# Optimization experiments

Hardware: AMD Instinct MI355X
Metric: run time of the kernel (lower is better)

Reference implementation:

```python
import jax, jax.numpy as jnp
import numpy as np

LRELU = 0.01
EPS = 1e-5
HEADS = 4


def _ln(x, g, b):
    m = x.mean(-1, keepdims=True)
    v = ((x - m) ** 2).mean(-1, keepdims=True)
    return (x - m) / jnp.sqrt(v + EPS) * g + b


def _mapx(x, w1, b1, g1, be1, w2, b2, g2, be2, w3, b3):
    h = jax.nn.leaky_relu(_ln(x @ w1 + b1, g1, be1), LRELU)
    h = jax.nn.leaky_relu(_ln(h @ w2 + b2, g2, be2), LRELU)
    return h @ w3 + b3


def _mcab(x, y, wq, bq, wk, bk, wv, bv, wo, bo, rescale):
    # spectral (channel-wise) multi-head cross attention: q from x, k/v from y
    b, c, h, w = x.shape
    n = h * w
    xt = x.reshape(b, c, n).transpose(0, 2, 1)  # (b, n, c)
    yt = y.reshape(b, c, n).transpose(0, 2, 1)
    dh = c // HEADS
    q = (xt @ wq + bq).reshape(b, n, HEADS, dh).transpose(0, 2, 3, 1)  # (b,H,dh,n)
    k = (yt @ wk + bk).reshape(b, n, HEADS, dh).transpose(0, 2, 3, 1)
    v = (yt @ wv + bv).reshape(b, n, HEADS, dh).transpose(0, 2, 3, 1)
    q = q / (jnp.linalg.norm(q, axis=-1, keepdims=True) + 1e-8)
    k = k / (jnp.linalg.norm(k, axis=-1, keepdims=True) + 1e-8)
    attn = jax.nn.softmax(jnp.einsum('bhdn,bhen->bhde', q, k) * rescale, axis=-1)  # (b,H,dh,dh)
    out = jnp.einsum('bhde,bhen->bhdn', attn, v)  # (b,H,dh,n)
    out = out.transpose(0, 3, 1, 2).reshape(b, n, c) @ wo + bo
    out = out + xt  # residual
    return out.transpose(0, 2, 1).reshape(b, c, h, w)


def setup_inputs() -> dict:
    key = jax.random.key(0)
    ks = jax.random.split(key, 16)
    B, C, H, W, K = 4, 64, 128, 128, 21
    s = 0.02
    nrm = lambda k, shape: jax.random.normal(k, shape, jnp.float32) * s
    return {
        'x': jax.random.normal(ks[0], (B, C, H, W), jnp.float32),
        'semantic': jax.random.uniform(ks[1], (B, K, H, W), jnp.float32),
        'wa': nrm(ks[2], (1, C, 4)), 'ba': jnp.zeros((1, 4), jnp.float32),
        'wb': nrm(ks[3], (20, C, 3)), 'bb': jnp.zeros((20, 3), jnp.float32),
        'in_w': nrm(ks[4], (C, C)), 'in_b': jnp.zeros((C,), jnp.float32),
        'mx_w1': nrm(ks[5], (C, 2 * C)), 'mx_b1': jnp.zeros((2 * C,), jnp.float32),
        'mx_g1': jnp.ones((2 * C,), jnp.float32), 'mx_be1': jnp.zeros((2 * C,), jnp.float32),
        'mx_w2': nrm(ks[6], (2 * C, 2 * C)), 'mx_b2': jnp.zeros((2 * C,), jnp.float32),
        'mx_g2': jnp.ones((2 * C,), jnp.float32), 'mx_be2': jnp.zeros((2 * C,), jnp.float32),
        'mx_w3': nrm(ks[7], (2 * C, C)), 'mx_b3': jnp.zeros((C,), jnp.float32),
        'wq': nrm(ks[8], (C, C)), 'bq': jnp.zeros((C,), jnp.float32),
        'wk': nrm(ks[9], (C, C)), 'bk': jnp.zeros((C,), jnp.float32),
        'wv': nrm(ks[10], (C, C)), 'bv': jnp.zeros((C,), jnp.float32),
        'wo': nrm(ks[11], (C, C)), 'bo': jnp.zeros((C,), jnp.float32),
        'rescale': jnp.ones((HEADS, 1, 1), jnp.float32),
    }


def reference(x, semantic, wa, ba, wb, bb, in_w, in_b,
              mx_w1, mx_b1, mx_g1, mx_be1, mx_w2, mx_b2, mx_g2, mx_be2,
              mx_w3, mx_b3, wq, bq, wk, bk, wv, bv, wo, bo, rescale):
    sem = jax.nn.relu(semantic)            # (b,K,h,w)
    xh = x.transpose(0, 2, 3, 1)           # (b,h,w,c)
    # per-class mask-multiply: (b,K,h,w,c)
    masked = xh[:, None] * sem[:, :, :, :, None]
    # class 0 gets the extra channel (64 = 1*4 + 20*3)
    feat_a = jnp.einsum('bkhwc,kcd->bkhwd', masked[:, :1], wa) + ba[None, :, None, None, :]
    feat_b = jnp.einsum('bkhwc,kcd->bkhwd', masked[:, 1:], wb) + bb[None, :, None, None, :]
    b, _, h, w, _ = feat_a.shape
    feat_a = feat_a.reshape(b, h, w, 4)
    feat_b = jnp.moveaxis(feat_b, 1, 3).reshape(b, h, w, 60)  # preserve class order
    all_feat = jnp.concatenate([feat_a, feat_b], axis=-1)     # (b,h,w,64)
    y = (all_feat @ in_w + in_b).transpose(0, 3, 1, 2)        # (b,c,h,w)
    xm = _mapx(xh, mx_w1, mx_b1, mx_g1, mx_be1, mx_w2, mx_b2, mx_g2, mx_be2, mx_w3, mx_b3)
    xm = xm.transpose(0, 3, 1, 2)
    return _mcab(xm, y, wq, bq, wk, bk, wv, bv, wo, bo, rescale)
```

## Files before the change

kernel.cpp:

```cpp
#include <hip/hip_runtime.h>
#include <hip/hip_bf16.h>

#define NPX 16384
typedef __attribute__((ext_vector_type(8))) short short8;
typedef __attribute__((ext_vector_type(8))) _Float16 half8;
typedef __attribute__((ext_vector_type(4))) float f32x4;

#define DEV static __device__ __forceinline__

#define WAB   0
#define WINW  4096
#define W1T   8192
#define W2T   16384
#define W3T   32768
#define WQT   40960
#define WKV   45056
#define WTOT  53248

DEV float lrelu(float v) { return v >= 0.f ? v : 0.01f * v; }
DEV short f2h(float f) { _Float16 h = (_Float16)f; return __builtin_bit_cast(short, h); }
DEV float h2f(short s) { return (float)__builtin_bit_cast(_Float16, s); }
DEV f32x4 mfmah(half8 a, half8 b, f32x4 c) {
    return __builtin_amdgcn_mfma_f32_16x16x32_f16(a, b, c, 0, 0, 0);
}

template<int K, int NT, int M>
DEV void gemmM(const short* __restrict__ A, int pitch,
               const short* __restrict__ WT, f32x4 (&acc)[M][NT])
{
    int lane = threadIdx.x & 63;
    int ln = lane & 15, q8 = (lane >> 4) * 8;
    const short* bp = WT + ln * K + q8;
#pragma unroll
    for (int c0 = 0; c0 < K; c0 += 32) {
        half8 a[M];
#pragma unroll
        for (int m = 0; m < M; ++m)
            a[m] = *(const half8*)(A + (size_t)(m * 16 + ln) * pitch + q8 + c0);
#pragma unroll
        for (int t = 0; t < NT; ++t) {
            half8 b = *(const half8*)(bp + (size_t)t * 16 * K + c0);
#pragma unroll
            for (int m = 0; m < M; ++m) acc[m][t] = mfmah(a[m], b, acc[m][t]);
        }
    }
}

template<int NT, int M>
DEV void acc_biasM(f32x4 (&acc)[M][NT], const float* __restrict__ bias)
{
    int ln = threadIdx.x & 15;
#pragma unroll
    for (int t = 0; t < NT; ++t) {
        float bv = bias[t * 16 + ln];
        f32x4 v = {bv, bv, bv, bv};
#pragma unroll
        for (int m = 0; m < M; ++m) acc[m][t] = v;
    }
}

template<int NT, int M>
DEV void dstoreM(const f32x4 (&acc)[M][NT], short* sD, int pitch)
{
    int lane = threadIdx.x & 63;
    int ln = lane & 15, r0 = (lane >> 4) * 4;
#pragma unroll
    for (int m = 0; m < M; ++m)
#pragma unroll
        for (int t = 0; t < NT; ++t)
#pragma unroll
            for (int r = 0; r < 4; ++r)
                sD[(m * 16 + r0 + r) * pitch + t * 16 + ln] = f2h(acc[m][t][r]);
}

template<int NT, int M>
DEV void ln_regM(f32x4 (&acc)[M][NT], const float* __restrict__ g, const float* __restrict__ be)
{
    int lane = threadIdx.x & 63, ln = lane & 15;
#pragma unroll
    for (int m = 0; m < M; ++m) {
        f32x4 s = {0,0,0,0}, ss = {0,0,0,0};
#pragma unroll
        for (int t = 0; t < NT; ++t)
#pragma unroll
            for (int r = 0; r < 4; ++r) { float v = acc[m][t][r]; s[r] += v; ss[r] += v * v; }
#pragma unroll
        for (int off = 1; off < 16; off <<= 1)
#pragma unroll
            for (int r = 0; r < 4; ++r) {
                s[r] += __shfl_xor(s[r], off);
                ss[r] += __shfl_xor(ss[r], off);
            }
        f32x4 mm, rs;
#pragma unroll
        for (int r = 0; r < 4; ++r) {
            float mean = s[r] * (1.f / 128.f);
            float var = ss[r] * (1.f / 128.f) - mean * mean;
            mm[r] = mean; rs[r] = rsqrtf(var + 1e-5f);
        }
#pragma unroll
        for (int t = 0; t < NT; ++t) {
            float gg = g[t * 16 + ln], bb = be[t * 16 + ln];
#pragma unroll
            for (int r = 0; r < 4; ++r)
                acc[m][t][r] = lrelu((acc[m][t][r] - mm[r]) * rs[r] * gg + bb);
        }
    }
}

template<int ROWS>
DEV void copyoutR(const short* sD, int pitch, short* __restrict__ dst)
{
    int lane = threadIdx.x & 63;
#pragma unroll
    for (int it = 0; it < ROWS / 8; ++it) {
        int idx = it * 512 + lane * 8;
        int px = idx >> 6, c = idx & 63;
        short8 v = *(const short8*)(&sD[px * pitch + c]);
        *reinterpret_cast<short8*>(dst + (size_t)px * 64 + c) = v;
    }
}

DEV void stage_x32(const float* __restrict__ xb, int n0, short* X)
{
    int lane = threadIdx.x & 63;
    int ln = lane & 15, qd = lane >> 4;
#pragma unroll
    for (int m = 0; m < 2; ++m) {
        float vb[16];
#pragma unroll
        for (int t = 0; t < 16; ++t)
            vb[t] = xb[(size_t)(qd * 16 + t) * NPX + n0 + m * 16 + ln];
        short8 lo, hi;
#pragma unroll
        for (int t = 0; t < 8; ++t) { lo[t] = f2h(vb[t]); hi[t] = f2h(vb[8 + t]); }
        *reinterpret_cast<short8*>(&X[(m * 16 + ln) * 72 + qd * 16]) = lo;
        *reinterpret_cast<short8*>(&X[(m * 16 + ln) * 72 + qd * 16 + 8]) = hi;
    }
}

__global__ __launch_bounds__(256) void k_prep(const float* __restrict__ wa,
                                              const float* __restrict__ wb,
                                              const float* __restrict__ in_w,
                                              const float* __restrict__ w1,
                                              const float* __restrict__ w2,
                                              const float* __restrict__ w3,
                                              const float* __restrict__ wq,
                                              const float* __restrict__ wk,
                                              const float* __restrict__ wv,
                                              short* __restrict__ wt)
{
    int idx = blockIdx.x * 256 + threadIdx.x;
    if (idx >= WTOT) return;
    float v;
    if (idx < WINW) {
        int j = idx >> 6, c = idx & 63;
        v = (j < 4) ? wa[c * 4 + j] : wb[((j - 4) / 3) * 192 + c * 3 + ((j - 4) % 3)];
    } else if (idx < W1T) {
        int i = idx - WINW; v = in_w[(i & 63) * 64 + (i >> 6)];
    } else if (idx < W2T) {
        int i = idx - W1T; v = w1[(i & 63) * 128 + (i >> 6)];
    } else if (idx < W3T) {
        int i = idx - W2T; v = w2[(i & 127) * 128 + (i >> 7)];
    } else if (idx < WQT) {
        int i = idx - W3T; v = w3[(i & 127) * 64 + (i >> 7)];
    } else if (idx < WKV) {
        int i = idx - WQT; v = wq[(i & 63) * 64 + (i >> 6)];
    } else {
        int i = idx - WKV; int e = i >> 6, k = i & 63;
        v = (e < 64) ? wk[k * 64 + e] : wv[k * 64 + (e - 64)];
    }
    wt[idx] = f2h(v);
}

__global__ __launch_bounds__(256) void k_fyk(const float* __restrict__ x,
                                             const float* __restrict__ sem,
                                             const float* __restrict__ ba,
                                             const float* __restrict__ bbv,
                                             const float* __restrict__ in_b,
                                             const float* __restrict__ bk,
                                             const float* __restrict__ bv,
                                             const short* __restrict__ wt,
                                             short* __restrict__ kout,
                                             short* __restrict__ vout)
{
    __shared__ short smem[4][3][32 * 72];
    int tid = threadIdx.x, w = tid >> 6, lane = tid & 63;
    int ln = lane & 15, qd = lane >> 4, r0 = qd * 4;
    int pw = blockIdx.x * 128 + w * 32;
    int b = pw >> 14, n0 = pw & (NPX - 1);
    const float* xb = x + (size_t)b * 64 * NPX;
    short* X  = smem[w][0];
    short* S1 = smem[w][1];
    short* S2 = smem[w][2];

    stage_x32(xb, n0, X);

    f32x4 a1[2][4];
    { f32x4 z = {0,0,0,0};
      for (int m = 0; m < 2; ++m) for (int t = 0; t < 4; ++t) a1[m][t] = z; }
    gemmM<64, 4, 2>(X, 72, wt + WAB, a1);
#pragma unroll
    for (int m = 0; m < 2; ++m)
#pragma unroll
        for (int t = 0; t < 4; ++t) {
            int j = t * 16 + ln;
            int cls = (j < 4) ? 0 : 1 + (j - 4) / 3;
            float bias = (j < 4) ? ba[j] : bbv[j - 4];
            f32x4 sm4 = *(const f32x4*)(sem + ((size_t)b * 21 + cls) * NPX + n0 + m * 16 + r0);
#pragma unroll
            for (int r = 0; r < 4; ++r)
                S1[(m * 16 + r0 + r) * 72 + j] = f2h(fmaxf(sm4[r], 0.f) * a1[m][t][r] + bias);
        }

    f32x4 a2[2][4];
    acc_biasM<4, 2>(a2, in_b);
    gemmM<64, 4, 2>(S1, 72, wt + WINW, a2);
    dstoreM<4, 2>(a2, S2, 72);

    f32x4 a3[2][8];
    {
#pragma unroll
        for (int t = 0; t < 8; ++t) {
            float bvv = (t < 4) ? bk[t * 16 + ln] : bv[(t - 4) * 16 + ln];
            f32x4 vv = {bvv, bvv, bvv, bvv};
            a3[0][t] = vv; a3[1][t] = vv;
        }
    }
    gemmM<64, 8, 2>(S2, 72, wt + WKV, a3);
#pragma unroll
    for (int m = 0; m < 2; ++m)
#pragma unroll
        for (int t = 0; t < 8; ++t)
#pragma unroll
            for (int r = 0; r < 4; ++r) {
                short hv = f2h(a3[m][t][r]);
                if (t < 4) S1[(m * 16 + r0 + r) * 72 + t * 16 + ln] = hv;
                else       X [(m * 16 + r0 + r) * 72 + (t - 4) * 16 + ln] = hv;
            }
    copyoutR<32>(S1, 72, kout + (size_t)pw * 64);
    copyoutR<32>(X, 72, vout + (size_t)pw * 64);
}

__global__ __launch_bounds__(256) void k_mlp(const float* __restrict__ x,
                                             const float* __restrict__ b1,
                                             const float* __restrict__ g1,
                                             const float* __restrict__ be1,
                                             const float* __restrict__ b2,
                                             const float* __restrict__ g2,
                                             const float* __restrict__ be2,
                                             const float* __restrict__ b3,
                                             const float* __restrict__ bq,
                                             const short* __restrict__ wt,
                                             short* __restrict__ xmout,
                                             short* __restrict__ qout)
{
    __shared__ short sX[4][32 * 72];
    __shared__ short sS[4][32 * 136];
    int tid = threadIdx.x, w = tid >> 6;
    int pw = blockIdx.x * 128 + w * 32;
    int b = pw >> 14, n0 = pw & (NPX - 1);
    const float* xb = x + (size_t)b * 64 * NPX;
    short* X = sX[w];
    short* S = sS[w];

    stage_x32(xb, n0, X);

    f32x4 acc[2][8];
    acc_biasM<8, 2>(acc, b1);
    gemmM<64, 8, 2>(X, 72, wt + W1T, acc);
    ln_regM<8, 2>(acc, g1, be1);
    dstoreM<8, 2>(acc, S, 136);

    acc_biasM<8, 2>(acc, b2);
    gemmM<128, 8, 2>(S, 136, wt + W2T, acc);
    ln_regM<8, 2>(acc, g2, be2);
    dstoreM<8, 2>(acc, S, 136);

    f32x4 a3[2][4];
    acc_biasM<4, 2>(a3, b3);
    gemmM<128, 4, 2>(S, 136, wt + W3T, a3);
    dstoreM<4, 2>(a3, X, 72);
    copyoutR<32>(X, 72, xmout + (size_t)pw * 64);

    f32x4 aq[2][4];
    acc_biasM<4, 2>(aq, bq);
    gemmM<64, 4, 2>(X, 72, wt + WQT, aq);
    dstoreM<4, 2>(aq, S, 136);
    copyoutR<32>(S, 136, qout + (size_t)pw * 64);
}

__global__ __launch_bounds__(256) void k_gram(const short* __restrict__ q,
                                              const short* __restrict__ k,
                                              float* __restrict__ gram,
                                              float* __restrict__ nsq)
{
    __shared__ short sQ[4][16 * 136], sK[4][16 * 136];
    int tid = threadIdx.x, w = tid >> 6, lane = tid & 63;
    int ln = lane & 15, q8 = (lane >> 4) * 8, qd = lane >> 4;
    int bh = blockIdx.x >> 5;
    int b = bh >> 2, h = bh & 3;
    int nb = (blockIdx.x & 31) * 512 + w * 128;
    size_t pxg = (size_t)b * NPX + nb;

#pragma unroll
    for (int it = 0; it < 4; ++it) {
        int idx = it * 64 + lane;
        int px = idx >> 1, half = idx & 1;
        short8 qv = *(const short8*)(q + (pxg + px) * 64 + h * 16 + half * 8);
        short8 kv = *(const short8*)(k + (pxg + px) * 64 + h * 16 + half * 8);
#pragma unroll
        for (int j = 0; j < 8; ++j) {
            sQ[w][(half * 8 + j) * 136 + px] = qv[j];
            sK[w][(half * 8 + j) * 136 + px] = kv[j];
        }
    }

    f32x4 aqk = {0,0,0,0}, aqq = {0,0,0,0}, akk = {0,0,0,0};
#pragma unroll
    for (int s = 0; s < 4; ++s) {
        half8 a  = *(const half8*)(&sQ[w][ln * 136 + s * 32 + q8]);
        half8 bb = *(const half8*)(&sK[w][ln * 136 + s * 32 + q8]);
        aqk = mfmah(a, bb, aqk);
        aqq = mfmah(a, a, aqq);
        akk = mfmah(bb, bb, akk);
    }
    int e = ln;
#pragma unroll
    for (int r = 0; r < 4; ++r) {
        int d = qd * 4 + r;
        atomicAdd(&gram[bh * 256 + d * 16 + e], aqk[r]);
        if (e == d) {
            atomicAdd(&nsq[bh * 16 + d], aqq[r]);
            atomicAdd(&nsq[256 + bh * 16 + d], akk[r]);
        }
    }
}

__global__ __launch_bounds__(256) void k_attnM(const float* __restrict__ gram,
                                               const float* __restrict__ nsq,
                                               const float* __restrict__ rescale,
                                               const float* __restrict__ wo,
                                               short* __restrict__ MT)
{
    __shared__ float s_at[1024];
    int b = blockIdx.x, tid = threadIdx.x;
    if (tid < 64) {
        int h = tid >> 4, d = tid & 15;
        float nq = sqrtf(nsq[b * 64 + h * 16 + d]) + 1e-8f;
        float rsc = rescale[h];
        float lg[16];
#pragma unroll
        for (int e = 0; e < 16; ++e) {
            float nk = sqrtf(nsq[256 + b * 64 + h * 16 + e]) + 1e-8f;
            lg[e] = rsc * gram[b * 1024 + h * 256 + d * 16 + e] / (nq * nk);
        }
        float m = lg[0];
#pragma unroll
        for (int e = 1; e < 16; ++e) m = fmaxf(m, lg[e]);
        float ssum = 0.f;
#pragma unroll
        for (int e = 0; e < 16; ++e) { lg[e] = expf(lg[e] - m); ssum += lg[e]; }
        float inv = 1.f / ssum;
#pragma unroll
        for (int e = 0; e < 16; ++e) s_at[h * 256 + d * 16 + e] = lg[e] * inv;
    }
    __syncthreads();
    int he = tid >> 2, h = he >> 4, e = he & 15;
    int cc0 = (tid & 3) * 16;
#pragma unroll
    for (int cx = 0; cx < 16; ++cx) {
        int cc = cc0 + cx;
        float s = 0.f;
#pragma unroll
        for (int d = 0; d < 16; ++d)
            s = fmaf(s_at[h * 256 + d * 16 + e], wo[(h * 16 + d) * 64 + cc], s);
        MT[b * 4096 + cc * 64 + he] = f2h(s);
    }
}

__global__ __launch_bounds__(256) void k_out(const short* __restrict__ v,
                                             const short* __restrict__ xm,
                                             const short* __restrict__ MT,
                                             const float* __restrict__ bo,
                                             float* __restrict__ out)
{
    int tid = threadIdx.x, w = tid >> 6, lane = tid & 63;
    int ln = lane & 15, qd = lane >> 4;
    int pw = blockIdx.x * 64 + w * 16;
    int b = pw >> 14, n0 = pw & (NPX - 1);

    f32x4 acc[1][4];
    acc_biasM<4, 1>(acc, bo);
    gemmM<64, 4, 1>(v + (size_t)pw * 64, 64, MT + b * 4096, acc);

#pragma unroll
    for (int t = 0; t < 4; ++t) {
        int c = t * 16 + ln;
        f32x4 o;
#pragma unroll
        for (int r = 0; r < 4; ++r)
            o[r] = acc[0][t][r] + h2f(xm[(size_t)(pw + qd * 4 + r) * 64 + c]);
        *reinterpret_cast<f32x4*>(out + ((size_t)b * 64 + c) * NPX + n0 + qd * 4) = o;
    }
}

extern "C" void kernel_launch(void* const* d_in, const int* in_sizes, int n_in,
                              void* d_out, int out_size, void* d_ws, size_t ws_size,
                              hipStream_t stream)
{
    const float* x    = (const float*)d_in[0];
    const float* sem  = (const float*)d_in[1];
    const float* wa   = (const float*)d_in[2];
    const float* ba   = (const float*)d_in[3];
    const float* wb   = (const float*)d_in[4];
    const float* bbv  = (const float*)d_in[5];
    const float* in_w = (const float*)d_in[6];
    const float* in_b = (const float*)d_in[7];
    const float* w1   = (const float*)d_in[8];
    const float* b1   = (const float*)d_in[9];
    const float* g1   = (const float*)d_in[10];
    const float* be1  = (const float*)d_in[11];
    const float* w2   = (const float*)d_in[12];
    const float* b2   = (const float*)d_in[13];
    const float* g2   = (const float*)d_in[14];
    const float* be2  = (const float*)d_in[15];
    const float* w3   = (const float*)d_in[16];
    const float* b3   = (const float*)d_in[17];
    const float* wq   = (const float*)d_in[18];
    const float* bq   = (const float*)d_in[19];
    const float* wk   = (const float*)d_in[20];
    const float* bk   = (const float*)d_in[21];
    const float* wv   = (const float*)d_in[22];
    const float* bv   = (const float*)d_in[23];
    const float* wo   = (const float*)d_in[24];
    const float* bo   = (const float*)d_in[25];
    const float* rescale = (const float*)d_in[26];

    char* wsb = (char*)d_ws;
    short* wt   = (short*)wsb;
    short* kpx  = (short*)(wsb + (1u << 20));
    short* vpx  = (short*)(wsb + (1u << 20) + (8u << 20));
    short* xmp  = (short*)(wsb + (1u << 20) + (16u << 20));
    short* qpx  = (short*)(wsb + (1u << 20) + (24u << 20));
    float* gram = (float*)(wsb + (1u << 20) + (32u << 20));
    float* nsq  = gram + 4096;
    short* MT   = (short*)(nsq + 512);

    dim3 blk(256);
    k_prep<<<dim3(208), blk, 0, stream>>>(wa, wb, in_w, w1, w2, w3, wq, wk, wv, wt);
    hipMemsetAsync(gram, 0, (4096 + 512) * sizeof(float), stream);
    k_fyk<<<dim3(512), blk, 0, stream>>>(x, sem, ba, bbv, in_b, bk, bv, wt, kpx, vpx);
    k_mlp<<<dim3(512), blk, 0, stream>>>(x, b1, g1, be1, b2, g2, be2, b3, bq, wt, xmp, qpx);
    k_gram<<<dim3(512), blk, 0, stream>>>(qpx, kpx, gram, nsq);
    k_attnM<<<dim3(4), blk, 0, stream>>>(gram, nsq, rescale, wo, MT);
    k_out<<<dim3(1024), blk, 0, stream>>>(vpx, xmp, MT, bo, (float*)d_out);
}
```

Before: 193.5 us.

## Fuse feature/KV and MLP/Q kernels into one kernel with 16-pixel wave tiles

Merges the two per-pixel kernels (semantic feature + K/V projection, and MLP + Q projection) into a single kernel, so the input x is read from global memory and staged to LDS once instead of twice. Each wave now handles 16 pixels instead of 32 and the grid doubles, which lowers register and LDS use per wave. The two independent GEMM chains are interleaved, which may help latency hiding. In exchange, weight fragments are reused across fewer pixels per wave and each wave does more varied work.

```diff
diff --git a/kernel.cpp b/kernel.cpp
--- a/kernel.cpp
+++ b/kernel.cpp
@@ -121,22 +121,18 @@
     }
 }
 
-DEV void stage_x32(const float* __restrict__ xb, int n0, short* X)
+DEV void stage_x16(const float* __restrict__ xb, int n0, short* X)
 {
     int lane = threadIdx.x & 63;
     int ln = lane & 15, qd = lane >> 4;
-#pragma unroll
-    for (int m = 0; m < 2; ++m) {
-        float vb[16];
-#pragma unroll
-        for (int t = 0; t < 16; ++t)
-            vb[t] = xb[(size_t)(qd * 16 + t) * NPX + n0 + m * 16 + ln];
-        short8 lo, hi;
-#pragma unroll
-        for (int t = 0; t < 8; ++t) { lo[t] = f2h(vb[t]); hi[t] = f2h(vb[8 + t]); }
-        *reinterpret_cast<short8*>(&X[(m * 16 + ln) * 72 + qd * 16]) = lo;
-        *reinterpret_cast<short8*>(&X[(m * 16 + ln) * 72 + qd * 16 + 8]) = hi;
-    }
+    float vb[16];
+#pragma unroll
+    for (int t = 0; t < 16; ++t) vb[t] = xb[(size_t)(qd * 16 + t) * NPX + n0 + ln];
+    short8 lo, hi;
+#pragma unroll
+    for (int t = 0; t < 8; ++t) { lo[t] = f2h(vb[t]); hi[t] = f2h(vb[8 + t]); }
+    *reinterpret_cast<short8*>(&X[ln * 72 + qd * 16]) = lo;
+    *reinterpret_cast<short8*>(&X[ln * 72 + qd * 16 + 8]) = hi;
 }
 
 __global__ __launch_bounds__(256) void k_prep(const float* __restrict__ wa,
@@ -173,121 +169,105 @@
     wt[idx] = f2h(v);
 }
 
-__global__ __launch_bounds__(256) void k_fyk(const float* __restrict__ x,
-                                             const float* __restrict__ sem,
-                                             const float* __restrict__ ba,
-                                             const float* __restrict__ bbv,
-                                             const float* __restrict__ in_b,
-                                             const float* __restrict__ bk,
-                                             const float* __restrict__ bv,
-                                             const short* __restrict__ wt,
-                                             short* __restrict__ kout,
-                                             short* __restrict__ vout)
-{
-    __shared__ short smem[4][3][32 * 72];
+__global__ __launch_bounds__(256) void k_main(const float* __restrict__ x,
+                                              const float* __restrict__ sem,
+                                              const float* __restrict__ ba,
+                                              const float* __restrict__ bbv,
+                                              const float* __restrict__ in_b,
+                                              const float* __restrict__ bk,
+                                              const float* __restrict__ bv,
+                                              const float* __restrict__ b1,
+                                              const float* __restrict__ g1,
+                                              const float* __restrict__ be1,
+                                              const float* __restrict__ b2,
+                                              const float* __restrict__ g2,
+                                              const float* __restrict__ be2,
+                                              const float* __restrict__ b3,
+                                              const float* __restrict__ bq,
+                                              const short* __restrict__ wt,
+                                              short* __restrict__ kout,
+                                              short* __restrict__ vout,
+                                              short* __restrict__ xmout,
+                                              short* __restrict__ qout)
+{
+    __shared__ short sX[4][16 * 72];
+    __shared__ short sF[4][16 * 72];
+    __shared__ short sS[4][16 * 136];
     int tid = threadIdx.x, w = tid >> 6, lane = tid & 63;
     int ln = lane & 15, qd = lane >> 4, r0 = qd * 4;
-    int pw = blockIdx.x * 128 + w * 32;
+    int pw = blockIdx.x * 64 + w * 16;
     int b = pw >> 14, n0 = pw & (NPX - 1);
     const float* xb = x + (size_t)b * 64 * NPX;
-    short* X  = smem[w][0];
-    short* S1 = smem[w][1];
-    short* S2 = smem[w][2];
-
-    stage_x32(xb, n0, X);
-
-    f32x4 a1[2][4];
-    { f32x4 z = {0,0,0,0};
-      for (int m = 0; m < 2; ++m) for (int t = 0; t < 4; ++t) a1[m][t] = z; }
-    gemmM<64, 4, 2>(X, 72, wt + WAB, a1);
-#pragma unroll
-    for (int m = 0; m < 2; ++m)
-#pragma unroll
-        for (int t = 0; t < 4; ++t) {
-            int j = t * 16 + ln;
-            int cls = (j < 4) ? 0 : 1 + (j - 4) / 3;
-            float bias = (j < 4) ? ba[j] : bbv[j - 4];
-            f32x4 sm4 = *(const f32x4*)(sem + ((size_t)b * 21 + cls) * NPX + n0 + m * 16 + r0);
-#pragma unroll
-            for (int r = 0; r < 4; ++r)
-                S1[(m * 16 + r0 + r) * 72 + j] = f2h(fmaxf(sm4[r], 0.f) * a1[m][t][r] + bias);
-        }
-
-    f32x4 a2[2][4];
-    acc_biasM<4, 2>(a2, in_b);
-    gemmM<64, 4, 2>(S1, 72, wt + WINW, a2);
-    dstoreM<4, 2>(a2, S2, 72);
-
-    f32x4 a3[2][8];
+    short* X = sX[w];
+    short* F = sF[w];
+    short* S = sS[w];
+
+    stage_x16(xb, n0, X);
+
+    f32x4 ah1[1][8];
+    acc_biasM<8, 1>(ah1, b1);
+    gemmM<64, 8, 1>(X, 72, wt + W1T, ah1);
+    f32x4 af[1][4];
+    { f32x4 z = {0,0,0,0}; for (int t = 0; t < 4; ++t) af[0][t] = z; }
+    gemmM<64, 4, 1>(X, 72, wt + WAB, af);
+
+#pragma unroll
+    for (int t = 0; t < 4; ++t) {
+        int j = t * 16 + ln;
+        int cls = (j < 4) ? 0 : 1 + (j - 4) / 3;
+        float bias = (j < 4) ? ba[j] : bbv[j - 4];
+        f32x4 sm4 = *(const f32x4*)(sem + ((size_t)b * 21 + cls) * NPX + n0 + r0);
+#pragma unroll
+        for (int r = 0; r < 4; ++r)
+            F[(r0 + r) * 72 + j] = f2h(fmaxf(sm4[r], 0.f) * af[0][t][r] + bias);
+    }
+    ln_regM<8, 1>(ah1, g1, be1);
+    dstoreM<8, 1>(ah1, S, 136);
+
+    f32x4 ay[1][4];
+    acc_biasM<4, 1>(ay, in_b);
+    gemmM<64, 4, 1>(F, 72, wt + WINW, ay);
+    f32x4 ah2[1][8];
+    acc_biasM<8, 1>(ah2, b2);
+    gemmM<128, 8, 1>(S, 136, wt + W2T, ah2);
+    dstoreM<4, 1>(ay, F, 72);
+    ln_regM<8, 1>(ah2, g2, be2);
+    dstoreM<8, 1>(ah2, S, 136);
+
+    f32x4 akv[1][8];
     {
 #pragma unroll
         for (int t = 0; t < 8; ++t) {
             float bvv = (t < 4) ? bk[t * 16 + ln] : bv[(t - 4) * 16 + ln];
             f32x4 vv = {bvv, bvv, bvv, bvv};
-            a3[0][t] = vv; a3[1][t] = vv;
-        }
-    }
-    gemmM<64, 8, 2>(S2, 72, wt + WKV, a3);
-#pragma unroll
-    for (int m = 0; m < 2; ++m)
-#pragma unroll
-        for (int t = 0; t < 8; ++t)
-#pragma unroll
-            for (int r = 0; r < 4; ++r) {
-                short hv = f2h(a3[m][t][r]);
-                if (t < 4) S1[(m * 16 + r0 + r) * 72 + t * 16 + ln] = hv;
-                else       X [(m * 16 + r0 + r) * 72 + (t - 4) * 16 + ln] = hv;
-            }
-    copyoutR<32>(S1, 72, kout + (size_t)pw * 64);
-    copyoutR<32>(X, 72, vout + (size_t)pw * 64);
-}
-
-__global__ __launch_bounds__(256) void k_mlp(const float* __restrict__ x,
-                                             const float* __restrict__ b1,
-                                             const float* __restrict__ g1,
-                                             const float* __restrict__ be1,
-                                             const float* __restrict__ b2,
-                                             const float* __restrict__ g2,
-                                             const float* __restrict__ be2,
-                                             const float* __restrict__ b3,
-                                             const float* __restrict__ bq,
-                                             const short* __restrict__ wt,
-                                             short* __restrict__ xmout,
-                                             short* __restrict__ qout)
-{
-    __shared__ short sX[4][32 * 72];
-    __shared__ short sS[4][32 * 136];
-    int tid = threadIdx.x, w = tid >> 6;
-    int pw = blockIdx.x * 128 + w * 32;
-    int b = pw >> 14, n0 = pw & (NPX - 1);
-    const float* xb = x + (size_t)b * 64 * NPX;
-    short* X = sX[w];
-    short* S = sS[w];
-
-    stage_x32(xb, n0, X);
-
-    f32x4 acc[2][8];
-    acc_biasM<8, 2>(acc, b1);
-    gemmM<64, 8, 2>(X, 72, wt + W1T, acc);
-    ln_regM<8, 2>(acc, g1, be1);
-    dstoreM<8, 2>(acc, S, 136);
-
-    acc_biasM<8, 2>(acc, b2);
-    gemmM<128, 8, 2>(S, 136, wt + W2T, acc);
-    ln_regM<8, 2>(acc, g2, be2);
-    dstoreM<8, 2>(acc, S, 136);
-
-    f32x4 a3[2][4];
-    acc_biasM<4, 2>(a3, b3);
-    gemmM<128, 4, 2>(S, 136, wt + W3T, a3);
-    dstoreM<4, 2>(a3, X, 72);
-    copyoutR<32>(X, 72, xmout + (size_t)pw * 64);
-
-    f32x4 aq[2][4];
-    acc_biasM<4, 2>(aq, bq);
-    gemmM<64, 4, 2>(X, 72, wt + WQT, aq);
-    dstoreM<4, 2>(aq, S, 136);
-    copyoutR<32>(S, 136, qout + (size_t)pw * 64);
+            akv[0][t] = vv;
+        }
+    }
+    gemmM<64, 8, 1>(F, 72, wt + WKV, akv);
+    f32x4 axm[1][4];
+    acc_biasM<4, 1>(axm, b3);
+    gemmM<128, 4, 1>(S, 136, wt + W3T, axm);
+
+#pragma unroll
+    for (int t = 0; t < 4; ++t)
+#pragma unroll
+        for (int r = 0; r < 4; ++r)
+            F[(r0 + r) * 72 + t * 16 + ln] = f2h(akv[0][t][r]);
+    copyoutR<16>(F, 72, kout + (size_t)pw * 64);
+#pragma unroll
+    for (int t = 0; t < 4; ++t)
+#pragma unroll
+        for (int r = 0; r < 4; ++r)
+            F[(r0 + r) * 72 + t * 16 + ln] = f2h(akv[0][t + 4][r]);
+    copyoutR<16>(F, 72, vout + (size_t)pw * 64);
+
+    dstoreM<4, 1>(axm, X, 72);
+    copyoutR<16>(X, 72, xmout + (size_t)pw * 64);
+    f32x4 aq[1][4];
+    acc_biasM<4, 1>(aq, bq);
+    gemmM<64, 4, 1>(X, 72, wt + WQT, aq);
+    dstoreM<4, 1>(aq, F, 72);
+    copyoutR<16>(F, 72, qout + (size_t)pw * 64);
 }
 
 __global__ __launch_bounds__(256) void k_gram(const short* __restrict__ q,
@@ -450,8 +430,9 @@
     dim3 blk(256);
     k_prep<<<dim3(208), blk, 0, stream>>>(wa, wb, in_w, w1, w2, w3, wq, wk, wv, wt);
     hipMemsetAsync(gram, 0, (4096 + 512) * sizeof(float), stream);
-    k_fyk<<<dim3(512), blk, 0, stream>>>(x, sem, ba, bbv, in_b, bk, bv, wt, kpx, vpx);
-    k_mlp<<<dim3(512), blk, 0, stream>>>(x, b1, g1, be1, b2, g2, be2, b3, bq, wt, xmp, qpx);
+    k_main<<<dim3(1024), blk, 0, stream>>>(x, sem, ba, bbv, in_b, bk, bv,
+                                           b1, g1, be1, b2, g2, be2, b3, bq,
+                                           wt, kpx, vpx, xmp, qpx);
     k_gram<<<dim3(512), blk, 0, stream>>>(qpx, kpx, gram, nsq);
     k_attnM<<<dim3(4), blk, 0, stream>>>(gram, nsq, rescale, wo, MT);
     k_out<<<dim3(1024), blk, 0, stream>>>(vpx, xmp, MT, bo, (float*)d_out);
```

Result: slower. 207.4 us (+7.2%).
